# Optimization experiments

Hardware: AMD Instinct MI355X
Metric: run time of the kernel (lower is better)

The kernel has to match this reference:

```python
import jax, jax.numpy as jnp
import numpy as np

B, S, D, MULT, K, EPS = 8, 2048, 512, 4, 9, 1e-6


def setup_inputs() -> dict:
    key = jax.random.key(0)
    ks = jax.random.split(key, 12)
    w = lambda k, shape, s=0.02: jax.random.normal(k, shape, dtype=jnp.float32) * s
    return dict(
        x=jax.random.normal(ks[0], (B, S, D), dtype=jnp.float32),
        g=jnp.ones((D,), jnp.float32),
        W1=w(ks[1], (D, D)), b1=jnp.zeros((D,), jnp.float32),
        W2=w(ks[2], (D, D)), b2=jnp.zeros((D,), jnp.float32),
        dw_w=w(ks[3], (D, D, K)), dw_b=jnp.zeros((D,), jnp.float32),
        pw_w=w(ks[4], (D, D, 1)), pw_b=jnp.zeros((D,), jnp.float32),
        Wi=w(ks[5], (D, D)), bi=jnp.zeros((D,), jnp.float32),
        Wr=w(ks[6], (D, D)), br=jnp.zeros((D,), jnp.float32),
        lam=jax.random.normal(ks[7], (D,), dtype=jnp.float32),
        Wm1=w(ks[8], (D, D * MULT)), bm1=jnp.zeros((D * MULT,), jnp.float32),
        Wm2=w(ks[9], (D * MULT, D)), bm2=jnp.zeros((D,), jnp.float32),
    )


def _rglru(x, Wi, bi, Wr, br, lam):
    # Griffin RG-LRU: h_t = a_t * h_{t-1} + sqrt(1 - a_t^2) * (i_t * x_t), h_0 = 0
    r = jax.nn.sigmoid(x @ Wr + br)                 # [B,S,D] recurrence gate
    i = jax.nn.sigmoid(x @ Wi + bi)                 # [B,S,D] input gate
    log_a = -8.0 * jax.nn.softplus(lam) * r         # [B,S,D]
    a = jnp.exp(log_a)
    b = jnp.sqrt(1.0 - jnp.exp(2.0 * log_a)) * (i * x)

    def combine(e1, e2):
        a1, b1 = e1
        a2, b2 = e2
        return (a1 * a2, a2 * b1 + b2)

    _, h = jax.lax.associative_scan(combine, (a, b), axis=1)
    return h


def _conv1d(x_cdS, w_oik, b_o, pad):
    y = jax.lax.conv_general_dilated(
        x_cdS, w_oik, window_strides=(1,), padding=[pad],
        dimension_numbers=("NCH", "OIH", "NCH"))
    return y + b_o[None, :, None]


def reference(x, g, W1, b1, W2, b2, dw_w, dw_b, pw_w, pw_b,
              Wi, bi, Wr, br, lam, Wm1, bm1, Wm2, bm2):
    scale = jnp.sqrt(jnp.float32(D))

    def rms(t):  # matches torch: x / (||x||_2 + eps) * sqrt(D) * g
        n = jnp.linalg.norm(t, axis=-1, keepdims=True) + EPS
        return t / n * scale * g

    skip = x
    xn = rms(x)
    l1 = xn @ W1 + b1                               # [B,S,D]
    l2 = xn @ W2 + b2                               # [B,S,D]
    c = jnp.transpose(l1, (0, 2, 1))                # [B,D,S]
    c = _conv1d(c, dw_w, dw_b, (K // 2, K // 2))    # 'same' padding, k=9
    c = _conv1d(c, pw_w, pw_b, (0, 0))              # pointwise k=1
    l1 = jnp.transpose(c, (0, 2, 1))                # [B,S,D]
    l1 = _rglru(l1, Wi, bi, Wr, br, lam)
    x1 = l1 * jax.nn.gelu(l2, approximate=False) + skip

    skip2 = x1
    xn2 = rms(x1)
    h = xn2 @ Wm1 + bm1                             # [B,S,4D]
    out = (jax.nn.gelu(h, approximate=False) * h) @ Wm2 + bm2 + skip2
    return out
```

## Files before the change

kernel.cpp:

```cpp
#include <hip/hip_runtime.h>
#include <hip/hip_bf16.h>

typedef unsigned short ushort_t;
typedef unsigned short vus8 __attribute__((ext_vector_type(8)));
typedef short vs8 __attribute__((ext_vector_type(8)));
typedef float vf4 __attribute__((ext_vector_type(4)));

#define D_DIM 512
#define S_LEN 2048
#define B_SZ 8
#define T_TOK 16384
#define NCH 64
#define CLEN 32
#define APAD_ROWS 16640

__device__ __forceinline__ float bf2f(ushort_t u) {
  union { unsigned int i; float f; } v;
  v.i = ((unsigned int)u) << 16;
  return v.f;
}
__device__ __forceinline__ ushort_t f2bf(float f) {
  union { float f; unsigned int i; } v;
  v.f = f;
  unsigned int r = v.i + 0x7fffu + ((v.i >> 16) & 1u);
  return (ushort_t)(r >> 16);
}
__device__ __forceinline__ float gelu_exact(float x) {
  return 0.5f * x * (1.0f + erff(x * 0.7071067811865475f));
}
__device__ __forceinline__ float gelu_fast(float x) {
  float x3 = x * x * x;
  float E = __expf(1.5957691216057308f * __builtin_fmaf(0.044715f, x3, x));
  float r = 1.f / (1.f + E);
  return __builtin_fmaf(-x, r, x);
}
__device__ __forceinline__ float ld_in(const void* p, size_t i, int fl) {
  return fl ? ((const float*)p)[i] : bf2f(((const ushort_t*)p)[i]);
}
__device__ __forceinline__ int dt_fl(const ushort_t* gdt) {
  return !(gdt[0] == 0x3F80 && gdt[1] == 0x3F80);
}
__device__ __forceinline__ void gld_lds16(const ushort_t* g, ushort_t* l) {
  __builtin_amdgcn_global_load_lds(
      (const __attribute__((address_space(1))) unsigned int*)g,
      (__attribute__((address_space(3))) unsigned int*)l, 16, 0, 0);
}

__device__ __forceinline__ void ab_compute(ushort_t rp, ushort_t ip, ushort_t xv,
                                           float sp8, float& a, float& b) {
  float r = 1.f / (1.f + expf(-bf2f(rp)));
  float ig = 1.f / (1.f + expf(-bf2f(ip)));
  float la = -sp8 * r;
  a = expf(la);
  b = sqrtf(fmaxf(0.f, -expm1f(2.f * la))) * ig * bf2f(xv);
}

#define NJOBS 27
struct PrepJobs {
  const void* src[NJOBS];
  ushort_t* dst[NJOBS];
  int R[NJOBS];
  int C[NJOBS];
  int mode[NJOBS];
  int start[NJOBS];
  const void* gsrc;
  int njobs;
};
__global__ void mega_prep(PrepJobs J, const ushort_t* __restrict__ gdt) {
  __shared__ ushort_t ts[32][33];
  int fl = dt_fl(gdt);
  int bid = blockIdx.x;
  int j = 0;
  while (j + 1 < J.njobs && bid >= J.start[j + 1]) j++;
  int tile = bid - J.start[j];
  const void* in = J.src[j];
  ushort_t* out = J.dst[j];
  int mode = J.mode[j];
  if (mode == 2 || mode == 4) {
    int n = J.R[j];
    int base = tile * 8192;
#pragma unroll 4
    for (int q = 0; q < 32; q++) {
      int i = base + q * 256 + threadIdx.x;
      if (i < n)
        out[i] = (mode == 4) ? (ushort_t)0
                             : (fl ? f2bf(((const float*)in)[i]) : ((const ushort_t*)in)[i]);
    }
    return;
  }
  int R = J.R[j], C = J.C[j];
  int tpr = C >> 5;
  int bc = tile % tpr, br = tile / tpr;
  int tx = threadIdx.x & 31, ty = threadIdx.x >> 5;
#pragma unroll
  for (int i = 0; i < 32; i += 8) {
    size_t idx = (size_t)(br * 32 + ty + i) * C + bc * 32 + tx;
    ts[ty + i][tx] = fl ? f2bf(((const float*)in)[idx]) : ((const ushort_t*)in)[idx];
  }
  __syncthreads();
#pragma unroll
  for (int i = 0; i < 32; i += 8) {
    int r = bc * 32 + ty + i;
    int orow = (mode == 1) ? (r % 9) * 512 + r / 9 : r;
    ushort_t val = ts[tx][ty + i];
    if (mode == 3) {
      int kcol = br * 32 + tx;
      val = f2bf(bf2f(val) * ld_in(J.gsrc, kcol, fl));
    }
    out[(size_t)orow * R + br * 32 + tx] = val;
  }
}

__global__ void gam_kernel(const ushort_t* __restrict__ tpw, const ushort_t* __restrict__ dwbc,
                           const ushort_t* __restrict__ pwbc, const ushort_t* __restrict__ lamc,
                           float* __restrict__ gam, float* __restrict__ sp8b) {
  int t = blockIdx.x * 256 + threadIdx.x;
  if (t < 512) {
    float l = bf2f(lamc[t]);
    sp8b[t] = 8.f * ((l > 20.f) ? l : log1pf(expf(l)));
  }
  int wave = threadIdx.x >> 6, lane = threadIdx.x & 63;
  int o = blockIdx.x * 4 + wave;
  vus8 v = *(const vus8*)(tpw + (size_t)o * 512 + lane * 8);
  vus8 w = *(const vus8*)(dwbc + lane * 8);
  float p = 0.f;
#pragma unroll
  for (int q = 0; q < 8; q++) p += bf2f(v[q]) * bf2f(w[q]);
#pragma unroll
  for (int off = 32; off; off >>= 1) p += __shfl_xor(p, off, 64);
  if (lane == 0) gam[o] = p + bf2f(pwbc[o]);
}

__global__ void rms_kernel(const void* __restrict__ x, const ushort_t* __restrict__ gdt,
                           const ushort_t* __restrict__ gc, ushort_t* __restrict__ out) {
  int fl = dt_fl(gdt);
  int wave = threadIdx.x >> 6, lane = threadIdx.x & 63;
  int row = blockIdx.x * 4 + wave;
  size_t base = (size_t)row * D_DIM + lane * 8;
  float f[8];
  float ss = 0.f;
#pragma unroll
  for (int j = 0; j < 8; j++) { f[j] = ld_in(x, base + j, fl); ss += f[j] * f[j]; }
#pragma unroll
  for (int off = 32; off > 0; off >>= 1) ss += __shfl_xor(ss, off, 64);
  float sc = 22.62741699796952f / (sqrtf(ss) + 1e-6f);
  vus8 o;
#pragma unroll
  for (int j = 0; j < 8; j++) o[j] = f2bf(f[j] * sc * bf2f(gc[lane * 8 + j]));
  *(vus8*)(out + base) = o;
}

template <int ACT>
__global__ __launch_bounds__(256, 2) void gemm_bt(
    const ushort_t* __restrict__ A, const ushort_t* __restrict__ Bt,
    const ushort_t* __restrict__ bias, void* __restrict__ Cv,
    const ushort_t* __restrict__ skip, const float* __restrict__ rowss,
    const ushort_t* __restrict__ gdt, int N, int K, int lda, int row0,
    size_t zsA, size_t zsB, size_t zsC) {
  __shared__ __align__(16) ushort_t As[128 * 32];
  __shared__ __align__(16) ushort_t Bs[128 * 32];
  A += (size_t)blockIdx.z * zsA;
  Bt += (size_t)blockIdx.z * zsB;
  const size_t zC = (size_t)blockIdx.z * zsC;
  const int tid = threadIdx.x;
  const int bm = blockIdx.y, bn = blockIdx.x;
  const int wave = tid >> 6, lane = tid & 63;
  const int wm = wave & 1, wn = wave >> 1;
  const int quad = lane >> 4, l16 = lane & 15;
  const int ofl = (ACT == 2) ? dt_fl(gdt) : 0;
  const int srow = wave * 32 + (lane >> 2);
  const int scol = (lane & 3) * 8;
  const ushort_t* gA = A + (size_t)(bm * 128 + srow) * lda + scol;
  const ushort_t* gB = Bt + (size_t)(bn * 128 + srow) * K + scol;
  ushort_t* lA0 = As + (wave * 32) * 32;
  ushort_t* lA1 = As + (wave * 32 + 16) * 32;
  ushort_t* lB0 = Bs + (wave * 32) * 32;
  ushort_t* lB1 = Bs + (wave * 32 + 16) * 32;
  vf4 acc[4][4] = {};
  for (int k0 = 0; k0 < K; k0 += 32) {
    __syncthreads();
    gld_lds16(gA + k0, lA0);
    gld_lds16(gA + k0 + (size_t)16 * lda, lA1);
    gld_lds16(gB + k0, lB0);
    gld_lds16(gB + k0 + (size_t)16 * K, lB1);
    __syncthreads();
    vs8 af[4], bfr[4];
#pragma unroll
    for (int mi = 0; mi < 4; mi++)
      af[mi] = *(const vs8*)(As + (wm * 64 + mi * 16 + l16) * 32 + quad * 8);
#pragma unroll
    for (int ni = 0; ni < 4; ni++)
      bfr[ni] = *(const vs8*)(Bs + (wn * 64 + ni * 16 + l16) * 32 + quad * 8);
#pragma unroll
    for (int mi = 0; mi < 4; mi++)
#pragma unroll
      for (int ni = 0; ni < 4; ni++)
        acc[mi][ni] =
            __builtin_amdgcn_mfma_f32_16x16x32_bf16(af[mi], bfr[ni], acc[mi][ni], 0, 0, 0);
  }
#pragma unroll
  for (int mi = 0; mi < 4; mi++) {
#pragma unroll
    for (int ni = 0; ni < 4; ni++) {
      int gcol = bn * 128 + wn * 64 + ni * 16 + l16;
      float bv = bias ? bf2f(bias[gcol]) : 0.f;
#pragma unroll
      for (int r = 0; r < 4; r++) {
        int grow = row0 + bm * 128 + wm * 64 + mi * 16 + quad * 4 + r;
        size_t oidx = zC + (size_t)grow * N + gcol;
        float v;
        if (ACT == 3) {
          float sc = 22.62741699796952f / (sqrtf(rowss[grow]) + 1e-6f);
          v = acc[mi][ni][r] * sc + bv;
          v = gelu_exact(v) * v;
        } else {
          v = acc[mi][ni][r] + bv;
        }
        if (ACT == 2) v += bf2f(skip[(size_t)grow * N + gcol]);
        if (ACT == 2 && ofl) ((float*)Cv)[oidx] = v;
        else ((ushort_t*)Cv)[oidx] = f2bf(v);
      }
    }
  }
}

template <int ACT>
__global__ __launch_bounds__(512, 2) void gemm256(
    const ushort_t* __restrict__ A, const ushort_t* __restrict__ Bt,
    const ushort_t* __restrict__ bias, ushort_t* __restrict__ C,
    const float* __restrict__ rowss, int N, int K) {
  __shared__ __align__(16) ushort_t lds[65536];
  const int tid = threadIdx.x;
  const int bn = blockIdx.x, bm = blockIdx.y;
  const int wave = tid >> 6, lane = tid & 63;
  const int wm = wave & 1, wn = wave >> 1;
  const int quad = lane >> 4, l16 = lane & 15;
  const int NT = K >> 5;

  const int r2 = tid >> 2;
  const int scol = (((tid & 3) ^ ((r2 >> 1) & 3)) << 3);
  const ushort_t* gA0 = A + (size_t)(bm * 256 + r2) * K + scol;
  const ushort_t* gB0 = Bt + (size_t)(bn * 256 + r2) * K + scol;
  const size_t hstep = (size_t)128 * K;
  ushort_t* ldsW = lds + (wave << 9);

  const int cA = ((quad ^ ((l16 >> 1) & 3)) << 3);

  vf4 acc[8][4] = {};

#define STAGE(t, slot)                            \
  do {                                            \
    const ushort_t* ga = gA0 + (t) * 32;          \
    const ushort_t* gb = gB0 + (t) * 32;          \
    ushort_t* d = ldsW + (slot) * 16384;          \
    gld_lds16(ga, d);                             \
    gld_lds16(ga + hstep, d + 4096);              \
    gld_lds16(gb, d + 8192);                      \
    gld_lds16(gb + hstep, d + 12288);             \
  } while (0)

  STAGE(0, 0);
  STAGE(1, 1);

  for (int t = 0; t < NT; ++t) {
    if (t + 1 < NT)
      asm volatile("s_waitcnt vmcnt(4)" ::: "memory");
    else
      asm volatile("s_waitcnt vmcnt(0)" ::: "memory");
    __builtin_amdgcn_s_barrier();
    __builtin_amdgcn_sched_barrier(0);
    if (t + 2 < NT) STAGE(t + 2, (t + 2) & 3);
    const ushort_t* L = lds + (t & 3) * 16384;
    vs8 af[8], bf[4];
#pragma unroll
    for (int mi = 0; mi < 8; mi++)
      af[mi] = *(const vs8*)(L + (wm * 128 + mi * 16 + l16) * 32 + cA);
#pragma unroll
    for (int ni = 0; ni < 4; ni++)
      bf[ni] = *(const vs8*)(L + 8192 + (wn * 64 + ni * 16 + l16) * 32 + cA);
    asm volatile("s_waitcnt lgkmcnt(0)" ::: "memory");
    __builtin_amdgcn_sched_barrier(0);
    __builtin_amdgcn_s_setprio(1);
#pragma unroll
    for (int mi = 0; mi < 8; mi++)
#pragma unroll
      for (int ni = 0; ni < 4; ni++)
        acc[mi][ni] =
            __builtin_amdgcn_mfma_f32_16x16x32_bf16(af[mi], bf[ni], acc[mi][ni], 0, 0, 0);
    __builtin_amdgcn_s_setprio(0);
    __builtin_amdgcn_sched_barrier(0);
  }
#undef STAGE

#pragma unroll
  for (int mi = 0; mi < 8; mi++) {
    const int growb = bm * 256 + wm * 128 + mi * 16 + quad * 4;
    float scv[4];
    if (ACT == 3) {
#pragma unroll
      for (int r = 0; r < 4; r++)
        scv[r] = 22.62741699796952f / (sqrtf(rowss[growb + r]) + 1e-6f);
    }
#pragma unroll
    for (int ni = 0; ni < 4; ni++) {
      const int gcol = bn * 256 + wn * 64 + ni * 16 + l16;
      const float bv = bf2f(bias[gcol]);
#pragma unroll
      for (int r = 0; r < 4; r++) {
        float v = acc[mi][ni][r];
        if (ACT == 3) {
          v = v * scv[r] + bv;
          v = gelu_fast(v) * v;
        } else {
          v += bv;
        }
        int grow = growb + r;
        size_t orow = (ACT == 1) ? (size_t)grow + (size_t)((grow >> 11) << 4) + 4
                                 : (size_t)grow;
        C[orow * N + gcol] = f2bf(v);
      }
    }
  }
}

__global__ __launch_bounds__(256, 2) void conv_p(
    const ushort_t* __restrict__ Apad, const ushort_t* __restrict__ Bt9,
    const float* __restrict__ gam, ushort_t* __restrict__ C) {
  __shared__ __align__(16) ushort_t Asl[2][4352];
  __shared__ __align__(16) ushort_t Bsl[2][12288];
  const int tid = threadIdx.x;
  const int bid = blockIdx.x;
  const int xid = bid & 7, cid = bid >> 3;
  const int bn = xid >> 1;
  const int bm = (xid & 1) * 64 + cid;
  const int batch = bm >> 4, seg = bm & 15;
  const int wave = tid >> 6, lane = tid & 63;
  const int wm = wave & 1, wn = wave >> 1;
  const int quad = lane >> 4, l16 = lane & 15;
  const int lr4 = lane >> 2;
  const int scg = (((lane & 3) ^ ((lane >> 3) & 3)) << 3);
  const int cB = ((quad ^ ((l16 >> 1) & 3)) << 3);
  const int bnc = bn * 128;
  const size_t arow0 = (size_t)batch * 2064 + seg * 128;
  const ushort_t* A0 = Apad + arow0 * 1024;
  vf4 acc[4][4] = {};

  auto stageA = [&](int k0, int s) {
    const ushort_t* src = A0 + (size_t)lr4 * 1024 + k0 * 32 + scg;
    ushort_t* dst = &Asl[s][0];
    gld_lds16(src + (size_t)(wave * 16) * 1024, dst + wave * 512);
    gld_lds16(src + (size_t)(64 + wave * 16) * 1024, dst + (64 + wave * 16) * 32);
    if (lane < 32) gld_lds16(src + (size_t)128 * 1024, dst + 128 * 32);
  };
  auto stageB = [&](int k0, int kg, int s) {
#pragma unroll
    for (int h = 0; h < 6; h++) {
      int m = h * 4 + wave;
      int kbl = m >> 3, r16 = m & 7;
      const ushort_t* gsrc = Bt9 +
          ((size_t)(kg * 3 + kbl) * D_DIM + bnc + r16 * 16 + lr4) * D_DIM + k0 * 32 + scg;
      gld_lds16(gsrc, &Bsl[s][0] + m * 512);
    }
  };

#define READF(KB, KBL)                                                            \
  do {                                                                            \
    int kb_ = (KB);                                                               \
    _Pragma("unroll") for (int mi = 0; mi < 4; mi++) {                            \
      int row = wm * 64 + mi * 16 + l16 + kb_;                                    \
      af[KBL][mi] = *(const vs8*)(LA + row * 32 + ((quad ^ ((row >> 1) & 3)) << 3)); \
    }                                                                             \
    _Pragma("unroll") for (int ni = 0; ni < 4; ni++)                              \
      bfr[KBL][ni] =                                                              \
          *(const vs8*)(LB + (KBL) * 4096 + (wn * 64 + ni * 16 + l16) * 32 + cB); \
  } while (0)

#define MFMACL(KBL)                                                               \
  do {                                                                            \
    __builtin_amdgcn_sched_barrier(0);                                            \
    __builtin_amdgcn_s_setprio(1);                                                \
    _Pragma("unroll") for (int mi = 0; mi < 4; mi++)                              \
      _Pragma("unroll") for (int ni = 0; ni < 4; ni++)                            \
        acc[mi][ni] = __builtin_amdgcn_mfma_f32_16x16x32_bf16(                    \
            af[KBL][mi], bfr[KBL][ni], acc[mi][ni], 0, 0, 0);                     \
    __builtin_amdgcn_s_setprio(0);                                                \
    __builtin_amdgcn_sched_barrier(0);                                            \
  } while (0)

#define CPH(K0, KG, LASTP)                                                        \
  do {                                                                            \
    asm volatile("s_waitcnt vmcnt(0)" ::: "memory");                              \
    __builtin_amdgcn_s_barrier();                                                 \
    __builtin_amdgcn_sched_barrier(0);                                            \
    if (!(LASTP)) {                                                               \
      int nk0 = (K0), nkg = (KG) + 1;                                             \
      if (nkg == 3) { nkg = 0; nk0++; }                                           \
      stageB(nk0, nkg, ((K0) * 3 + (KG) + 1) & 1);                                \
      if ((KG) == 1 && (K0) + 1 < 16) stageA((K0) + 1, ((K0) + 1) & 1);           \
    }                                                                             \
    __builtin_amdgcn_sched_barrier(0);                                            \
    const ushort_t* LA = &Asl[(K0) & 1][0];                                       \
    const ushort_t* LB = &Bsl[((K0) * 3 + (KG)) & 1][0];                          \
    vs8 af[3][4], bfr[3][4];                                                      \
    READF((KG) * 3 + 0, 0);                                                       \
    READF((KG) * 3 + 1, 1);                                                       \
    __builtin_amdgcn_sched_barrier(0);                                            \
    asm volatile("s_waitcnt lgkmcnt(8)" ::: "memory");                            \
    MFMACL(0);                                                                    \
    READF((KG) * 3 + 2, 2);                                                       \
    __builtin_amdgcn_sched_barrier(0);                                            \
    asm volatile("s_waitcnt lgkmcnt(8)" ::: "memory");                            \
    MFMACL(1);                                                                    \
    asm volatile("s_waitcnt lgkmcnt(0)" ::: "memory");                            \
    MFMACL(2);                                                                    \
  } while (0)

  stageA(0, 0);
  stageB(0, 0, 0);
  for (int k0 = 0; k0 < 16; ++k0) {
    CPH(k0, 0, false);
    CPH(k0, 1, false);
    CPH(k0, 2, k0 == 15);
  }
#undef CPH
#undef MFMACL
#undef READF

#pragma unroll
  for (int mi = 0; mi < 4; mi++) {
#pragma unroll
    for (int ni = 0; ni < 4; ni++) {
      int gcol = bnc + wn * 64 + ni * 16 + l16;
      float gv = gam[gcol];
#pragma unroll
      for (int r = 0; r < 4; r++) {
        int grow = bm * 128 + wm * 64 + mi * 16 + quad * 4 + r;
        C[(size_t)grow * D_DIM + gcol] = f2bf(acc[mi][ni][r] + gv);
      }
    }
  }
}

__global__ void scan_pass1(const ushort_t* __restrict__ P, const ushort_t* __restrict__ xin,
                           const float* __restrict__ sp8b, float* __restrict__ Aagg,
                           float* __restrict__ Bagg) {
  int bid = blockIdx.x;
  int dblk = bid & 1, c = (bid >> 1) & (NCH - 1), bb = bid >> 7;
  int d = dblk * 256 + threadIdx.x;
  float sp8 = sp8b[d];
  size_t baseP = ((size_t)bb * S_LEN + c * CLEN) * 1024 + d;
  size_t baseX = ((size_t)bb * S_LEN + c * CLEN) * D_DIM + d;
  float Ap = 1.f, h = 0.f;
  for (int s = 0; s < CLEN; s++) {
    float av, bv;
    ab_compute(P[baseP + (size_t)s * 1024], P[baseP + 512 + (size_t)s * 1024],
               xin[baseX + (size_t)s * D_DIM], sp8, av, bv);
    Ap *= av;
    h = av * h + bv;
  }
  size_t o = ((size_t)bb * NCH + c) * D_DIM + d;
  Aagg[o] = Ap;
  Bagg[o] = h;
}

__global__ void scan_carry(const float* __restrict__ Aagg, const float* __restrict__ Bagg,
                           float* __restrict__ carry) {
  int idx = blockIdx.x * 256 + threadIdx.x;
  int bb = idx >> 9, d = idx & (D_DIM - 1);
  float h = 0.f;
  for (int c = 0; c < NCH; c++) {
    size_t o = ((size_t)bb * NCH + c) * D_DIM + d;
    carry[o] = h;
    h = Aagg[o] * h + Bagg[o];
  }
}

__global__ void scan_pass2(const ushort_t* __restrict__ P, const float* __restrict__ sp8b,
                           const float* __restrict__ carry, const ushort_t* __restrict__ l2p,
                           const void* __restrict__ x, const ushort_t* __restrict__ gdt,
                           ushort_t* xio, float* __restrict__ rowss) {
  int fl = dt_fl(gdt);
  int bid = blockIdx.x;
  int dblk = bid & 1, c = (bid >> 1) & (NCH - 1), bb = bid >> 7;
  int d = dblk * 256 + threadIdx.x;
  int lane = threadIdx.x & 63;
  float sp8 = sp8b[d];
  float h = carry[((size_t)bb * NCH + c) * D_DIM + d];
  size_t baseP = ((size_t)bb * S_LEN + c * CLEN) * 1024 + d;
  size_t baseL = ((size_t)bb * 2064 + 4 + c * CLEN) * 1024 + 512 + d;
  size_t base = ((size_t)bb * S_LEN + c * CLEN) * D_DIM + d;
  int row0 = bb * S_LEN + c * CLEN;
  for (int s = 0; s < CLEN; s++) {
    size_t idx = base + (size_t)s * D_DIM;
    float av, bv;
    ab_compute(P[baseP + (size_t)s * 1024], P[baseP + 512 + (size_t)s * 1024], xio[idx], sp8,
               av, bv);
    h = av * h + bv;
    float l2v = bf2f(l2p[baseL + (size_t)s * 1024]);
    float xv = ld_in(x, idx, fl);
    float v = h * gelu_fast(l2v) + xv;
    xio[idx] = f2bf(v);
    float p = v * v;
#pragma unroll
    for (int o2 = 32; o2; o2 >>= 1) p += __shfl_xor(p, o2, 64);
    if (lane == 0) atomicAdd(&rowss[row0 + s], p);
  }
}

extern "C" void kernel_launch(void* const* d_in, const int* in_sizes, int n_in, void* d_out,
                              int out_size, void* d_ws, size_t ws_size, hipStream_t stream) {
  (void)in_sizes; (void)n_in; (void)out_size; (void)ws_size;
  const void* x   = d_in[0];
  const void* g   = d_in[1];
  const void* W1  = d_in[2];
  const void* b1  = d_in[3];
  const void* W2  = d_in[4];
  const void* b2  = d_in[5];
  const void* dww = d_in[6];
  const void* dwb = d_in[7];
  const void* pww = d_in[8];
  const void* pwb = d_in[9];
  const void* Wi  = d_in[10];
  const void* bi  = d_in[11];
  const void* Wr  = d_in[12];
  const void* br  = d_in[13];
  const void* lam = d_in[14];
  const void* Wm1 = d_in[15];
  const void* bm1 = d_in[16];
  const void* Wm2 = d_in[17];
  const void* bm2 = d_in[18];
  const ushort_t* gdt = (const ushort_t*)g;

  char* ws = (char*)d_ws;
  size_t off = 0;
  auto take = [&](size_t n) {
    void* p = ws + off;
    off += (n + 255) & ~(size_t)255;
    return p;
  };
  const size_t ACT_B = (size_t)T_TOK * D_DIM * 2;
  ushort_t* tW12 = (ushort_t*)take((size_t)1024 * 512 * 2);
  ushort_t* tWri = (ushort_t*)take((size_t)1024 * 512 * 2);
  ushort_t* tWm1 = (ushort_t*)take((size_t)2048 * 512 * 2);
  ushort_t* tWm2 = (ushort_t*)take((size_t)2048 * 512 * 2);
  ushort_t* Wp   = (ushort_t*)take((size_t)9 * 512 * 512 * 2);
  ushort_t* gc   = (ushort_t*)take(512 * 2);
  ushort_t* lamc = (ushort_t*)take(512 * 2);
  ushort_t* b12c = (ushort_t*)take(1024 * 2);
  ushort_t* bric = (ushort_t*)take(1024 * 2);
  ushort_t* bm2c = (ushort_t*)take(512 * 2);
  ushort_t* bm1c = (ushort_t*)take(2048 * 2);
  ushort_t* dwbc = (ushort_t*)take(512 * 2);
  ushort_t* pwbc = (ushort_t*)take(512 * 2);
  float* gam     = (float*)take(512 * 4);
  float* sp8b    = (float*)take(512 * 4);
  float* rowss   = (float*)take((size_t)T_TOK * 4);
  ushort_t* Apad2 = (ushort_t*)take((size_t)APAD_ROWS * 1024 * 2);
  ushort_t* PriB  = (ushort_t*)take((size_t)T_TOK * 1024 * 2);
  ushort_t* S4    = (ushort_t*)take(ACT_B);
  float* Aagg  = (float*)take((size_t)B_SZ * NCH * D_DIM * 4);
  float* Bagg  = (float*)take((size_t)B_SZ * NCH * D_DIM * 4);
  float* carry = (float*)take((size_t)B_SZ * NCH * D_DIM * 4);
  ushort_t* tpw  = PriB;
  ushort_t* tdwT = PriB + 262144;
  ushort_t* u    = Apad2;

  hipMemsetAsync(rowss, 0, (size_t)T_TOK * 4, stream);

  PrepJobs J;
  const void* js[NJOBS] = {g, lam, b1, b2, dwb, pwb, br, bi, bm2, bm1, pww,
                           W1, W2, Wr, Wi, Wm1, Wm2, dww,
                           nullptr, nullptr, nullptr, nullptr, nullptr, nullptr, nullptr,
                           nullptr, nullptr};
  ushort_t* jd[NJOBS] = {gc, lamc, b12c, b12c + 512, dwbc, pwbc, bric, bric + 512, bm2c, bm1c,
                         tpw, tW12, tW12 + (size_t)512 * 512, tWri, tWri + (size_t)512 * 512,
                         tWm1, tWm2, tdwT,
                         Apad2,
                         Apad2 + (size_t)(0 * 2064 + 2052) * 1024,
                         Apad2 + (size_t)(1 * 2064 + 2052) * 1024,
                         Apad2 + (size_t)(2 * 2064 + 2052) * 1024,
                         Apad2 + (size_t)(3 * 2064 + 2052) * 1024,
                         Apad2 + (size_t)(4 * 2064 + 2052) * 1024,
                         Apad2 + (size_t)(5 * 2064 + 2052) * 1024,
                         Apad2 + (size_t)(6 * 2064 + 2052) * 1024,
                         Apad2 + (size_t)(7 * 2064 + 2052) * 1024};
  int jR[NJOBS] = {512, 512, 512, 512, 512, 512, 512, 512, 512, 2048, 262144,
                   512, 512, 512, 512, 512, 2048, 512,
                   4096, 16384, 16384, 16384, 16384, 16384, 16384, 16384, 12288};
  int jC[NJOBS] = {0, 0, 0, 0, 0, 0, 0, 0, 0, 0, 0, 512, 512, 512, 512, 2048, 512, 4608,
                   0, 0, 0, 0, 0, 0, 0, 0, 0};
  int jm[NJOBS] = {2, 2, 2, 2, 2, 2, 2, 2, 2, 2, 2, 0, 0, 0, 0, 3, 0, 1,
                   4, 4, 4, 4, 4, 4, 4, 4, 4};
  int cum = 0;
  for (int i = 0; i < NJOBS; i++) {
    J.src[i] = js[i]; J.dst[i] = jd[i]; J.R[i] = jR[i]; J.C[i] = jC[i]; J.mode[i] = jm[i];
    J.start[i] = cum;
    cum += (jm[i] == 2 || jm[i] == 4) ? (jR[i] + 8191) / 8192 : (jC[i] / 32) * (jR[i] / 32);
  }
  J.gsrc = g;
  J.njobs = NJOBS;
  mega_prep<<<cum, 256, 0, stream>>>(J, gdt);
  gemm_bt<0><<<dim3(4, 4, 9), 256, 0, stream>>>(tpw, tdwT, nullptr, Wp, nullptr, nullptr, gdt,
                                                512, 512, 512, 0, 0, (size_t)512 * 512,
                                                (size_t)512 * 512);
  gam_kernel<<<128, 256, 0, stream>>>(tpw, dwbc, pwbc, lamc, gam, sp8b);

  rms_kernel<<<T_TOK / 4, 256, 0, stream>>>(x, gdt, gc, S4);
  gemm256<1><<<dim3(4, 64), 512, 0, stream>>>(S4, tW12, b12c, Apad2, nullptr, 1024, 512);
  conv_p<<<512, 256, 0, stream>>>(Apad2, Wp, gam, S4);
  gemm256<0><<<dim3(4, 64), 512, 0, stream>>>(S4, tWri, bric, PriB, nullptr, 1024, 512);
  scan_pass1<<<B_SZ * NCH * 2, 256, 0, stream>>>(PriB, S4, sp8b, Aagg, Bagg);
  scan_carry<<<16, 256, 0, stream>>>(Aagg, Bagg, carry);
  scan_pass2<<<B_SZ * NCH * 2, 256, 0, stream>>>(PriB, sp8b, carry, Apad2, x, gdt, S4, rowss);

  gemm256<3><<<dim3(8, 64), 512, 0, stream>>>(S4, tWm1, bm1c, u, rowss, 2048, 512);
  gemm_bt<2><<<dim3(4, 128), 256, 0, stream>>>(u, tWm2, bm2c, d_out, S4, nullptr, gdt, 512,
                                               2048, 2048, 0, 0, 0, 0);
}
```

Measured before the change: 501.7 us.

## Replace final down-projection GEMM with pipelined 256x128 swizzled-LDS kernel

Adds a new gemm256d kernel for the final Wm2 projection (K=2048). It uses a 256x128 tile, a 4-slot LDS ring with loads issued two stages ahead, swizzled LDS columns, explicit waitcnt/barrier scheduling and setprio around the MFMA block. The old kernel used a 128x128 tile with a single buffer synchronised twice per k-step. The fused bias+skip epilogue is moved into the new kernel and the unused ACT branches are stripped from gemm_bt. Separately, scan_carry is relaunched as 64 blocks of 64 threads instead of 16 blocks of 256 to spread the serial carry scan across more CUs.

```diff
diff --git a/kernel.cpp b/kernel.cpp
--- a/kernel.cpp
+++ b/kernel.cpp
@@ -167,7 +167,6 @@
   const int wave = tid >> 6, lane = tid & 63;
   const int wm = wave & 1, wn = wave >> 1;
   const int quad = lane >> 4, l16 = lane & 15;
-  const int ofl = (ACT == 2) ? dt_fl(gdt) : 0;
   const int srow = wave * 32 + (lane >> 2);
   const int scol = (lane & 3) * 8;
   const ushort_t* gA = A + (size_t)(bm * 128 + srow) * lda + scol;
@@ -208,17 +207,7 @@
       for (int r = 0; r < 4; r++) {
         int grow = row0 + bm * 128 + wm * 64 + mi * 16 + quad * 4 + r;
         size_t oidx = zC + (size_t)grow * N + gcol;
-        float v;
-        if (ACT == 3) {
-          float sc = 22.62741699796952f / (sqrtf(rowss[grow]) + 1e-6f);
-          v = acc[mi][ni][r] * sc + bv;
-          v = gelu_exact(v) * v;
-        } else {
-          v = acc[mi][ni][r] + bv;
-        }
-        if (ACT == 2) v += bf2f(skip[(size_t)grow * N + gcol]);
-        if (ACT == 2 && ofl) ((float*)Cv)[oidx] = v;
-        else ((ushort_t*)Cv)[oidx] = f2bf(v);
+        ((ushort_t*)Cv)[oidx] = f2bf(acc[mi][ni][r] + bv);
       }
     }
   }
@@ -318,6 +307,92 @@
         size_t orow = (ACT == 1) ? (size_t)grow + (size_t)((grow >> 11) << 4) + 4
                                  : (size_t)grow;
         C[orow * N + gcol] = f2bf(v);
+      }
+    }
+  }
+}
+
+__global__ __launch_bounds__(512, 2) void gemm256d(
+    const ushort_t* __restrict__ A, const ushort_t* __restrict__ Bt,
+    const ushort_t* __restrict__ bias, void* __restrict__ Cv,
+    const ushort_t* __restrict__ skip, const ushort_t* __restrict__ gdt,
+    int N, int K) {
+  __shared__ __align__(16) ushort_t lds[49152];
+  const int tid = threadIdx.x;
+  const int bn = blockIdx.x, bm = blockIdx.y;
+  const int wave = tid >> 6, lane = tid & 63;
+  const int wm = wave >> 1, wn = wave & 1;
+  const int quad = lane >> 4, l16 = lane & 15;
+  const int NT = K >> 5;
+  const int ofl = dt_fl(gdt);
+
+  const int r2 = tid >> 2;
+  const int scol = (((tid & 3) ^ ((r2 >> 1) & 3)) << 3);
+  const ushort_t* gA0 = A + (size_t)(bm * 256 + r2) * K + scol;
+  const ushort_t* gB0 = Bt + (size_t)(bn * 128 + r2) * K + scol;
+  const size_t hstep = (size_t)128 * K;
+  ushort_t* ldsW = lds + (wave << 9);
+
+  const int cA = ((quad ^ ((l16 >> 1) & 3)) << 3);
+
+  vf4 acc[4][4] = {};
+
+#define STAGE(t, slot)                            \
+  do {                                            \
+    const ushort_t* ga = gA0 + (t) * 32;          \
+    ushort_t* d = ldsW + (slot) * 12288;          \
+    gld_lds16(ga, d);                             \
+    gld_lds16(ga + hstep, d + 4096);              \
+    gld_lds16(gB0 + (t) * 32, d + 8192);          \
+  } while (0)
+
+  STAGE(0, 0);
+  STAGE(1, 1);
+
+  for (int t = 0; t < NT; ++t) {
+    if (t + 1 < NT)
+      asm volatile("s_waitcnt vmcnt(3)" ::: "memory");
+    else
+      asm volatile("s_waitcnt vmcnt(0)" ::: "memory");
+    __builtin_amdgcn_s_barrier();
+    __builtin_amdgcn_sched_barrier(0);
+    if (t + 2 < NT) STAGE(t + 2, (t + 2) & 3);
+    const ushort_t* L = lds + (t & 3) * 12288;
+    vs8 af[4], bf[4];
+#pragma unroll
+    for (int mi = 0; mi < 4; mi++)
+      af[mi] = *(const vs8*)(L + (wm * 64 + mi * 16 + l16) * 32 + cA);
+#pragma unroll
+    for (int ni = 0; ni < 4; ni++)
+      bf[ni] = *(const vs8*)(L + 8192 + (wn * 64 + ni * 16 + l16) * 32 + cA);
+    asm volatile("s_waitcnt lgkmcnt(0)" ::: "memory");
+    __builtin_amdgcn_sched_barrier(0);
+    __builtin_amdgcn_s_setprio(1);
+#pragma unroll
+    for (int mi = 0; mi < 4; mi++)
+#pragma unroll
+      for (int ni = 0; ni < 4; ni++)
+        acc[mi][ni] =
+            __builtin_amdgcn_mfma_f32_16x16x32_bf16(af[mi], bf[ni], acc[mi][ni], 0, 0, 0);
+    __builtin_amdgcn_s_setprio(0);
+    __builtin_amdgcn_sched_barrier(0);
+  }
+#undef STAGE
+
+#pragma unroll
+  for (int mi = 0; mi < 4; mi++) {
+    const int growb = bm * 256 + wm * 64 + mi * 16 + quad * 4;
+#pragma unroll
+    for (int ni = 0; ni < 4; ni++) {
+      const int gcol = bn * 128 + wn * 64 + ni * 16 + l16;
+      const float bv = bf2f(bias[gcol]);
+#pragma unroll
+      for (int r = 0; r < 4; r++) {
+        const int grow = growb + r;
+        const size_t oidx = (size_t)grow * N + gcol;
+        float v = acc[mi][ni][r] + bv + bf2f(skip[oidx]);
+        if (ofl) ((float*)Cv)[oidx] = v;
+        else ((ushort_t*)Cv)[oidx] = f2bf(v);
       }
     }
   }
@@ -465,7 +540,7 @@
 
 __global__ void scan_carry(const float* __restrict__ Aagg, const float* __restrict__ Bagg,
                            float* __restrict__ carry) {
-  int idx = blockIdx.x * 256 + threadIdx.x;
+  int idx = blockIdx.x * 64 + threadIdx.x;
   int bb = idx >> 9, d = idx & (D_DIM - 1);
   float h = 0.f;
   for (int c = 0; c < NCH; c++) {
@@ -610,10 +685,9 @@
   conv_p<<<512, 256, 0, stream>>>(Apad2, Wp, gam, S4);
   gemm256<0><<<dim3(4, 64), 512, 0, stream>>>(S4, tWri, bric, PriB, nullptr, 1024, 512);
   scan_pass1<<<B_SZ * NCH * 2, 256, 0, stream>>>(PriB, S4, sp8b, Aagg, Bagg);
-  scan_carry<<<16, 256, 0, stream>>>(Aagg, Bagg, carry);
+  scan_carry<<<64, 64, 0, stream>>>(Aagg, Bagg, carry);
   scan_pass2<<<B_SZ * NCH * 2, 256, 0, stream>>>(PriB, sp8b, carry, Apad2, x, gdt, S4, rowss);
 
   gemm256<3><<<dim3(8, 64), 512, 0, stream>>>(S4, tWm1, bm1c, u, rowss, 2048, 512);
-  gemm_bt<2><<<dim3(4, 128), 256, 0, stream>>>(u, tWm2, bm2c, d_out, S4, nullptr, gdt, 512,
-                                               2048, 2048, 0, 0, 0, 0);
-}
+  gemm256d<<<dim3(4, 64), 512, 0, stream>>>(u, tWm2, bm2c, d_out, S4, gdt, 512, 2048);
+}
```

Result: faster. 480.9 us (-4.1%).

## Switch GEMMs to 256x128 tiles, route final GEMM through pipelined kernel

Applied to the files above, without the earlier changes.

The 256x256 pipelined GEMM becomes a 256x128 variant with 8 waves in a 4x2 layout and a smaller LDS ring. This doubles the grid for the W12, Wri and Wm1 GEMMs, which should improve CU occupancy and tail balance. The final Wm2 GEMM with the skip add now also runs on this pipelined kernel instead of the simpler 128x128 gemm_bt. Separately, the RG-LRU gate math uses fast __expf with 1-exp instead of expm1, which loses some precision for small arguments. scan_carry is also relaunched with 64 threads per block across more blocks.

```diff
diff --git a/kernel.cpp b/kernel.cpp
--- a/kernel.cpp
+++ b/kernel.cpp
@@ -48,11 +48,11 @@
 
 __device__ __forceinline__ void ab_compute(ushort_t rp, ushort_t ip, ushort_t xv,
                                            float sp8, float& a, float& b) {
-  float r = 1.f / (1.f + expf(-bf2f(rp)));
-  float ig = 1.f / (1.f + expf(-bf2f(ip)));
+  float r = 1.f / (1.f + __expf(-bf2f(rp)));
+  float ig = 1.f / (1.f + __expf(-bf2f(ip)));
   float la = -sp8 * r;
-  a = expf(la);
-  b = sqrtf(fmaxf(0.f, -expm1f(2.f * la))) * ig * bf2f(xv);
+  a = __expf(la);
+  b = sqrtf(fmaxf(0.f, 1.f - __expf(2.f * la))) * ig * bf2f(xv);
 }
 
 #define NJOBS 27
@@ -167,7 +167,6 @@
   const int wave = tid >> 6, lane = tid & 63;
   const int wm = wave & 1, wn = wave >> 1;
   const int quad = lane >> 4, l16 = lane & 15;
-  const int ofl = (ACT == 2) ? dt_fl(gdt) : 0;
   const int srow = wave * 32 + (lane >> 2);
   const int scol = (lane & 3) * 8;
   const ushort_t* gA = A + (size_t)(bm * 128 + srow) * lda + scol;
@@ -208,55 +207,45 @@
       for (int r = 0; r < 4; r++) {
         int grow = row0 + bm * 128 + wm * 64 + mi * 16 + quad * 4 + r;
         size_t oidx = zC + (size_t)grow * N + gcol;
-        float v;
-        if (ACT == 3) {
-          float sc = 22.62741699796952f / (sqrtf(rowss[grow]) + 1e-6f);
-          v = acc[mi][ni][r] * sc + bv;
-          v = gelu_exact(v) * v;
-        } else {
-          v = acc[mi][ni][r] + bv;
-        }
-        if (ACT == 2) v += bf2f(skip[(size_t)grow * N + gcol]);
-        if (ACT == 2 && ofl) ((float*)Cv)[oidx] = v;
-        else ((ushort_t*)Cv)[oidx] = f2bf(v);
+        ((ushort_t*)Cv)[oidx] = f2bf(acc[mi][ni][r] + bv);
       }
     }
   }
 }
 
 template <int ACT>
-__global__ __launch_bounds__(512, 2) void gemm256(
+__global__ __launch_bounds__(512, 2) void gemm128(
     const ushort_t* __restrict__ A, const ushort_t* __restrict__ Bt,
-    const ushort_t* __restrict__ bias, ushort_t* __restrict__ C,
-    const float* __restrict__ rowss, int N, int K) {
-  __shared__ __align__(16) ushort_t lds[65536];
+    const ushort_t* __restrict__ bias, void* __restrict__ Cv,
+    const ushort_t* __restrict__ skip, const float* __restrict__ rowss,
+    const ushort_t* __restrict__ gdt, int N, int K) {
+  __shared__ __align__(16) ushort_t lds[49152];
   const int tid = threadIdx.x;
   const int bn = blockIdx.x, bm = blockIdx.y;
   const int wave = tid >> 6, lane = tid & 63;
-  const int wm = wave & 1, wn = wave >> 1;
+  const int wm = wave >> 1, wn = wave & 1;
   const int quad = lane >> 4, l16 = lane & 15;
   const int NT = K >> 5;
+  const int ofl = (ACT == 2) ? dt_fl(gdt) : 0;
 
   const int r2 = tid >> 2;
   const int scol = (((tid & 3) ^ ((r2 >> 1) & 3)) << 3);
   const ushort_t* gA0 = A + (size_t)(bm * 256 + r2) * K + scol;
-  const ushort_t* gB0 = Bt + (size_t)(bn * 256 + r2) * K + scol;
+  const ushort_t* gB0 = Bt + (size_t)(bn * 128 + r2) * K + scol;
   const size_t hstep = (size_t)128 * K;
   ushort_t* ldsW = lds + (wave << 9);
 
   const int cA = ((quad ^ ((l16 >> 1) & 3)) << 3);
 
-  vf4 acc[8][4] = {};
+  vf4 acc[4][4] = {};
 
 #define STAGE(t, slot)                            \
   do {                                            \
     const ushort_t* ga = gA0 + (t) * 32;          \
-    const ushort_t* gb = gB0 + (t) * 32;          \
-    ushort_t* d = ldsW + (slot) * 16384;          \
+    ushort_t* d = ldsW + (slot) * 12288;          \
     gld_lds16(ga, d);                             \
     gld_lds16(ga + hstep, d + 4096);              \
-    gld_lds16(gb, d + 8192);                      \
-    gld_lds16(gb + hstep, d + 12288);             \
+    gld_lds16(gB0 + (t) * 32, d + 8192);          \
   } while (0)
 
   STAGE(0, 0);
@@ -264,17 +253,17 @@
 
   for (int t = 0; t < NT; ++t) {
     if (t + 1 < NT)
-      asm volatile("s_waitcnt vmcnt(4)" ::: "memory");
+      asm volatile("s_waitcnt vmcnt(3)" ::: "memory");
     else
       asm volatile("s_waitcnt vmcnt(0)" ::: "memory");
     __builtin_amdgcn_s_barrier();
     __builtin_amdgcn_sched_barrier(0);
     if (t + 2 < NT) STAGE(t + 2, (t + 2) & 3);
-    const ushort_t* L = lds + (t & 3) * 16384;
-    vs8 af[8], bf[4];
-#pragma unroll
-    for (int mi = 0; mi < 8; mi++)
-      af[mi] = *(const vs8*)(L + (wm * 128 + mi * 16 + l16) * 32 + cA);
+    const ushort_t* L = lds + (t & 3) * 12288;
+    vs8 af[4], bf[4];
+#pragma unroll
+    for (int mi = 0; mi < 4; mi++)
+      af[mi] = *(const vs8*)(L + (wm * 64 + mi * 16 + l16) * 32 + cA);
 #pragma unroll
     for (int ni = 0; ni < 4; ni++)
       bf[ni] = *(const vs8*)(L + 8192 + (wn * 64 + ni * 16 + l16) * 32 + cA);
@@ -282,7 +271,7 @@
     __builtin_amdgcn_sched_barrier(0);
     __builtin_amdgcn_s_setprio(1);
 #pragma unroll
-    for (int mi = 0; mi < 8; mi++)
+    for (int mi = 0; mi < 4; mi++)
 #pragma unroll
       for (int ni = 0; ni < 4; ni++)
         acc[mi][ni] =
@@ -293,8 +282,8 @@
 #undef STAGE
 
 #pragma unroll
-  for (int mi = 0; mi < 8; mi++) {
-    const int growb = bm * 256 + wm * 128 + mi * 16 + quad * 4;
+  for (int mi = 0; mi < 4; mi++) {
+    const int growb = bm * 256 + wm * 64 + mi * 16 + quad * 4;
     float scv[4];
     if (ACT == 3) {
 #pragma unroll
@@ -303,10 +292,11 @@
     }
 #pragma unroll
     for (int ni = 0; ni < 4; ni++) {
-      const int gcol = bn * 256 + wn * 64 + ni * 16 + l16;
+      const int gcol = bn * 128 + wn * 64 + ni * 16 + l16;
       const float bv = bf2f(bias[gcol]);
 #pragma unroll
       for (int r = 0; r < 4; r++) {
+        const int grow = growb + r;
         float v = acc[mi][ni][r];
         if (ACT == 3) {
           v = v * scv[r] + bv;
@@ -314,10 +304,16 @@
         } else {
           v += bv;
         }
-        int grow = growb + r;
         size_t orow = (ACT == 1) ? (size_t)grow + (size_t)((grow >> 11) << 4) + 4
                                  : (size_t)grow;
-        C[orow * N + gcol] = f2bf(v);
+        size_t oidx = orow * N + gcol;
+        if (ACT == 2) {
+          v += bf2f(skip[oidx]);
+          if (ofl) ((float*)Cv)[oidx] = v;
+          else ((ushort_t*)Cv)[oidx] = f2bf(v);
+        } else {
+          ((ushort_t*)Cv)[oidx] = f2bf(v);
+        }
       }
     }
   }
@@ -465,7 +461,7 @@
 
 __global__ void scan_carry(const float* __restrict__ Aagg, const float* __restrict__ Bagg,
                            float* __restrict__ carry) {
-  int idx = blockIdx.x * 256 + threadIdx.x;
+  int idx = blockIdx.x * 64 + threadIdx.x;
   int bb = idx >> 9, d = idx & (D_DIM - 1);
   float h = 0.f;
   for (int c = 0; c < NCH; c++) {
@@ -606,14 +602,17 @@
   gam_kernel<<<128, 256, 0, stream>>>(tpw, dwbc, pwbc, lamc, gam, sp8b);
 
   rms_kernel<<<T_TOK / 4, 256, 0, stream>>>(x, gdt, gc, S4);
-  gemm256<1><<<dim3(4, 64), 512, 0, stream>>>(S4, tW12, b12c, Apad2, nullptr, 1024, 512);
+  gemm128<1><<<dim3(8, 64), 512, 0, stream>>>(S4, tW12, b12c, Apad2, nullptr, nullptr, gdt,
+                                              1024, 512);
   conv_p<<<512, 256, 0, stream>>>(Apad2, Wp, gam, S4);
-  gemm256<0><<<dim3(4, 64), 512, 0, stream>>>(S4, tWri, bric, PriB, nullptr, 1024, 512);
+  gemm128<0><<<dim3(8, 64), 512, 0, stream>>>(S4, tWri, bric, PriB, nullptr, nullptr, gdt,
+                                              1024, 512);
   scan_pass1<<<B_SZ * NCH * 2, 256, 0, stream>>>(PriB, S4, sp8b, Aagg, Bagg);
-  scan_carry<<<16, 256, 0, stream>>>(Aagg, Bagg, carry);
+  scan_carry<<<64, 64, 0, stream>>>(Aagg, Bagg, carry);
   scan_pass2<<<B_SZ * NCH * 2, 256, 0, stream>>>(PriB, sp8b, carry, Apad2, x, gdt, S4, rowss);
 
-  gemm256<3><<<dim3(8, 64), 512, 0, stream>>>(S4, tWm1, bm1c, u, rowss, 2048, 512);
-  gemm_bt<2><<<dim3(4, 128), 256, 0, stream>>>(u, tWm2, bm2c, d_out, S4, nullptr, gdt, 512,
-                                               2048, 2048, 0, 0, 0, 0);
-}
+  gemm128<3><<<dim3(16, 64), 512, 0, stream>>>(S4, tWm1, bm1c, u, nullptr, rowss, gdt,
+                                               2048, 512);
+  gemm128<2><<<dim3(4, 64), 512, 0, stream>>>(u, tWm2, bm2c, d_out, S4, nullptr, gdt,
+                                              512, 2048);
+}
```

After: 473.7 us. -5.6%, faster.
